# Performance work log

Hardware: AMD Instinct MI355X
Metric: run time of the kernel (lower is better)

Reference implementation:

```python
import jax, jax.numpy as jnp
import numpy as np

B, V, M, H = 256, 128, 256, 1024
TIMING_DIM = 10          # ceil(log2(max_timesteps=1024))
DECAY_ALPHA = 0.99
IN_DIM = (V + TIMING_DIM + 1 + 1) * M  # 35840


def setup_inputs() -> dict:
    key = jax.random.key(0)
    ks = jax.random.split(key, 12)
    x = jax.random.uniform(ks[0], (B, V), dtype=jnp.float32)
    memory = jax.random.uniform(ks[1], (B, M, V), dtype=jnp.float32)
    memory_timings = jax.random.randint(ks[2], (B, M), 0, 1000).astype(jnp.int64)
    memory_surprise = jax.random.uniform(ks[3], (B, M), dtype=jnp.float32)
    last_prediction = jax.random.uniform(ks[4], (B, V), dtype=jnp.float32)
    s1 = 1.0 / np.sqrt(IN_DIM)
    s2 = 1.0 / np.sqrt(H)
    W1 = jax.random.uniform(ks[5], (IN_DIM, H), dtype=jnp.float32, minval=-s1, maxval=s1)
    b1 = jnp.zeros((H,), jnp.float32)
    Wg = jax.random.uniform(ks[6], (IN_DIM, H), dtype=jnp.float32, minval=-s1, maxval=s1)
    bg = jnp.zeros((H,), jnp.float32)
    W2 = jax.random.uniform(ks[7], (H, V), dtype=jnp.float32, minval=-s2, maxval=s2)
    b2 = jnp.zeros((V,), jnp.float32)
    return {"x": x, "memory": memory, "memory_timings": memory_timings,
            "memory_surprise": memory_surprise, "last_prediction": last_prediction,
            "W1": W1, "b1": b1, "Wg": Wg, "bg": bg, "W2": W2, "b2": b2}


def _step(x, memory, memory_timings, memory_surprise, last_prediction):
    # surprise of incoming token under last prediction
    surprise = -jnp.log(jnp.sum(x * last_prediction, axis=1) + 1e-8)  # [B]
    # age + decay
    timings = memory_timings + 1
    surp = memory_surprise * DECAY_ALPHA
    # ring-buffer roll, write newest at slot 0
    mem = jnp.roll(memory, 1, axis=1).at[:, 0, :].set(x)
    timings = jnp.roll(timings, 1, axis=1).at[:, 0].set(0)
    surp = jnp.roll(surp, 1, axis=1).at[:, 0].set(surprise)
    # sort by age ascending, gather memory/surprise
    idx = jnp.argsort(timings, axis=1)                               # [B,M]
    sorted_timings = jnp.take_along_axis(timings, idx, axis=1)       # [B,M]
    sorted_memory = jnp.take_along_axis(mem, idx[..., None], axis=1)  # [B,M,V]
    sorted_surprise = jnp.take_along_axis(surp, idx, axis=1)          # [B,M]
    # binary encode timings
    powers = 2 ** jnp.arange(TIMING_DIM, dtype=sorted_timings.dtype)
    bits = ((sorted_timings[..., None] // powers) % 2).astype(jnp.float32)  # [B,M,T]
    norm_t = sorted_timings.astype(jnp.float32) / (
        jnp.max(sorted_timings, axis=1, keepdims=True).astype(jnp.float32) + 1.0)
    pred_input = jnp.concatenate(
        [sorted_memory.reshape(B, -1), bits.reshape(B, -1),
         norm_t.reshape(B, -1), sorted_surprise.reshape(B, -1)], axis=1)  # [B, IN_DIM]
    return pred_input


def reference(x, memory, memory_timings, memory_surprise, last_prediction,
              W1, b1, Wg, bg, W2, b2):
    pred_input = _step(x, memory, memory_timings, memory_surprise, last_prediction)
    # gated dense network: h = (xW1+b1) * sigmoid(xWg+bg); logits = hW2+b2
    h = (pred_input @ W1 + b1) * jax.nn.sigmoid(pred_input @ Wg + bg)
    return h @ W2 + b2
```

## Files before the change

kernel.cpp:

```cpp
#include <hip/hip_runtime.h>
#include <stdint.h>
#include <math.h>

#define BB 256
#define VV 128
#define MM 256
#define TDIM 10
#define HH 1024
#define IN_DIM 35840
#define KSPLIT 16
#define KSLICE 2240
#define BK 64
#define NCHUNK 35

using f32x4  = __attribute__((ext_vector_type(4))) float;
using bf16x8 = __attribute__((ext_vector_type(8))) short;

__device__ __forceinline__ unsigned short f2bf(float f) {
    unsigned int u = __float_as_uint(f);
    unsigned int r = (u + 0x7FFFu + ((u >> 16) & 1u)) >> 16;
    return (unsigned short)r;
}

__device__ __forceinline__ void gload_lds16(const void* g, void* l) {
    __builtin_amdgcn_global_load_lds(
        (const __attribute__((address_space(1))) unsigned int*)g,
        (__attribute__((address_space(3))) unsigned int*)l,
        16, 0, 0);
}

__global__ __launch_bounds__(256)
void k_build(const float* __restrict__ x, const float* __restrict__ memory,
             const int* __restrict__ timings, const float* __restrict__ msurp,
             const float* __restrict__ lastp, short* __restrict__ A)
{
    int b = blockIdx.x, t = threadIdx.x;
    __shared__ int t_s[MM], idx_s[MM], st_s[MM];
    __shared__ float red[MM];
    __shared__ float s_surprise;

    t_s[t] = (t == 0) ? 0 : timings[b*MM + t - 1] + 1;
    red[t] = (t < VV) ? x[b*VV + t] * lastp[b*VV + t] : 0.f;
    __syncthreads();
    for (int s = 128; s > 0; s >>= 1) {
        if (t < s) red[t] += red[t + s];
        __syncthreads();
    }
    if (t == 0) s_surprise = -logf(red[0] + 1e-8f);

    int ti = t_s[t], cnt = 0;
    #pragma unroll 4
    for (int j = 0; j < MM; ++j) {
        int tj = t_s[j];
        cnt += (tj < ti) || (tj == ti && j < t);
    }
    idx_s[cnt] = t;
    st_s[cnt]  = ti;
    __syncthreads();

    float invm = 1.f / ((float)st_s[MM-1] + 1.f);
    short* Ab = A + (size_t)b * IN_DIM;
    {
        int st = st_s[t], src = idx_s[t];
        #pragma unroll
        for (int tt = 0; tt < TDIM; ++tt)
            Ab[32768 + t*TDIM + tt] = (short)f2bf((float)((st >> tt) & 1));
        Ab[35328 + t] = (short)f2bf((float)st * invm);
        float sv = (src == 0) ? s_surprise : msurp[b*MM + src - 1] * 0.99f;
        Ab[35584 + t] = (short)f2bf(sv);
    }
    int half = t >> 7, v = t & (VV-1);
    for (int p = half; p < MM; p += 2) {
        int src = idx_s[p];
        float val = (src == 0) ? x[b*VV + v]
                               : memory[((size_t)b*MM + src - 1)*VV + v];
        Ab[p*VV + v] = (short)f2bf(val);
    }
}

__global__ __launch_bounds__(256)
void k_gemm(const short* __restrict__ A, const float* __restrict__ W1,
            const float* __restrict__ Wg, float* __restrict__ P)
{
    int ks = blockIdx.x;
    int xt = blockIdx.y;
    const float* W = (xt < 16) ? W1 : Wg;
    int wcol0 = (xt & 15) * 64;
    int pcol0 = xt * 64;
    int k0 = ks * KSLICE;

    __shared__ bf16x8 As8[2048];
    __shared__ bf16x8 Ws8[512];

    int t = threadIdx.x;
    int l = t & 63, wv = t >> 6;
    int r = l & 15, q = l >> 4;

    int aoff[4][2], boff[4][2];
    #pragma unroll
    for (int mt = 0; mt < 4; ++mt)
        #pragma unroll
        for (int s = 0; s < 2; ++s)
            aoff[mt][s] = (wv*64 + mt*16 + r)*8 + ((q + 4*s) ^ (r & 7));
    #pragma unroll
    for (int nt = 0; nt < 4; ++nt)
        #pragma unroll
        for (int s = 0; s < 2; ++s)
            boff[nt][s] = (nt*16 + r)*8 + ((q + 4*s) ^ (r & 7));

    f32x4 acc[4][4];
    #pragma unroll
    for (int mt = 0; mt < 4; ++mt)
        #pragma unroll
        for (int nt = 0; nt < 4; ++nt)
            acc[mt][nt] = (f32x4){0.f, 0.f, 0.f, 0.f};

    int wn  = t & 63;
    int wq4 = t >> 6;

    for (int c = 0; c < NCHUNK; ++c) {
        int kc = k0 + c*BK;
        __syncthreads();
        #pragma unroll
        for (int i = 0; i < 8; ++i) {
            int G = t + i*256;
            int m = G >> 3;
            int kb = (G & 7) ^ (m & 7);
            const short* gp = A + (size_t)m*IN_DIM + kc + kb*8;
            gload_lds16(gp, (void*)(As8 + ((t & ~63) + i*256)));
        }
        #pragma unroll
        for (int p4 = 0; p4 < 4; ++p4) {
            int kbase = p4*16 + wq4*4;
            const float* wp = W + (size_t)(kc + kbase)*HH + wcol0 + wn;
            float w0 = wp[0], w1 = wp[HH], w2 = wp[2*HH], w3 = wp[3*HH];
            unsigned int lo = (unsigned int)f2bf(w0) | ((unsigned int)f2bf(w1) << 16);
            unsigned int hi = (unsigned int)f2bf(w2) | ((unsigned int)f2bf(w3) << 16);
            int kb = kbase >> 3, hf = (kbase >> 2) & 1;
            unsigned int* dst = (unsigned int*)((short*)Ws8 +
                                ((wn*8 + (kb ^ (wn & 7)))*8 + hf*4));
            dst[0] = lo; dst[1] = hi;
        }
        __syncthreads();

        #pragma unroll
        for (int s = 0; s < 2; ++s) {
            bf16x8 af[4], bfr[4];
            #pragma unroll
            for (int mt = 0; mt < 4; ++mt) af[mt] = As8[aoff[mt][s]];
            #pragma unroll
            for (int nt = 0; nt < 4; ++nt) bfr[nt] = Ws8[boff[nt][s]];
            #pragma unroll
            for (int mt = 0; mt < 4; ++mt)
                #pragma unroll
                for (int nt = 0; nt < 4; ++nt)
                    acc[mt][nt] = __builtin_amdgcn_mfma_f32_16x16x32_bf16(
                        af[mt], bfr[nt], acc[mt][nt], 0, 0, 0);
        }
    }

    #pragma unroll
    for (int mt = 0; mt < 4; ++mt)
        #pragma unroll
        for (int nt = 0; nt < 4; ++nt)
            #pragma unroll
            for (int rg = 0; rg < 4; ++rg) {
                int m = wv*64 + mt*16 + q*4 + rg;
                int n = pcol0 + nt*16 + r;
                P[((size_t)ks*BB + m)*2048 + n] = acc[mt][nt][rg];
            }
}

__global__ __launch_bounds__(256)
void k_reduce(const float* __restrict__ P, const float* __restrict__ b1,
              const float* __restrict__ bg, float* __restrict__ h)
{
    int id = blockIdx.x * 256 + threadIdx.x;
    int b = id >> 10, j = id & 1023;
    float p1 = b1[j], pg = bg[j];
    #pragma unroll
    for (int ks = 0; ks < KSPLIT; ++ks) {
        size_t base = ((size_t)ks*BB + b)*2048;
        p1 += P[base + j];
        pg += P[base + 1024 + j];
    }
    float g = 1.f / (1.f + expf(-pg));
    h[(size_t)b*HH + j] = p1 * g;
}

__global__ __launch_bounds__(512)
void k_out(const float* __restrict__ h, const float* __restrict__ W2,
           const float* __restrict__ b2, float* __restrict__ out)
{
    int t = threadIdx.x;
    int v = t & 127, bi = t >> 7;
    int b = blockIdx.x * 4 + bi;
    const float* hb = h + (size_t)b*HH;
    float acc = b2[v];
    #pragma unroll 8
    for (int k = 0; k < HH; ++k)
        acc += hb[k] * W2[k*VV + v];
    out[(size_t)b*VV + v] = acc;
}

extern "C" void kernel_launch(void* const* d_in, const int* in_sizes, int n_in,
                              void* d_out, int out_size, void* d_ws, size_t ws_size,
                              hipStream_t stream)
{
    const float* x    = (const float*)d_in[0];
    const float* mem  = (const float*)d_in[1];
    const int*   tim  = (const int*)d_in[2];
    const float* msur = (const float*)d_in[3];
    const float* lp   = (const float*)d_in[4];
    const float* W1   = (const float*)d_in[5];
    const float* b1   = (const float*)d_in[6];
    const float* Wg   = (const float*)d_in[7];
    const float* bg   = (const float*)d_in[8];
    const float* W2   = (const float*)d_in[9];
    const float* b2   = (const float*)d_in[10];
    float* out = (float*)d_out;

    short* A = (short*)d_ws;
    float* P = (float*)((char*)d_ws + 18350080);
    float* h = (float*)((char*)d_ws + 51904512);

    k_build <<<256, 256, 0, stream>>>(x, mem, tim, msur, lp, A);
    k_gemm  <<<dim3(KSPLIT, 32), 256, 0, stream>>>(A, W1, Wg, P);
    k_reduce<<<1024, 256, 0, stream>>>(P, b1, bg, h);
    k_out   <<<64, 512, 0, stream>>>(h, W2, b2, out);
}
```

Measured before the change: 446.7 us.

## Narrow GEMM N-tile, prefetch weights into registers, split output GEMV over K

The main GEMM tile drops from 64 to 32 output columns, doubling the grid to 1024 blocks for more occupancy (launch_bounds now asks for 4 blocks per CU). Weight loads for the next K-chunk are issued into registers before the barrier, so global fp32 weight reads overlap with compute; each thread now loads 8 consecutive K rows and writes one 16-byte LDS vector. The A tile is now re-read from global twice as often because each block covers fewer columns. The final h@W2 kernel runs one block per batch row and splits K across two halves, combining them through shared memory, so the GEMV is spread over more blocks.

Result: no change. 439.6 us (-1.6%).

```diff
diff --git a/kernel.cpp b/kernel.cpp
--- a/kernel.cpp
+++ b/kernel.cpp
@@ -78,49 +78,61 @@
     }
 }
 
-__global__ __launch_bounds__(256)
+__global__ __launch_bounds__(256, 4)
 void k_gemm(const short* __restrict__ A, const float* __restrict__ W1,
             const float* __restrict__ Wg, float* __restrict__ P)
 {
     int ks = blockIdx.x;
     int xt = blockIdx.y;
-    const float* W = (xt < 16) ? W1 : Wg;
-    int wcol0 = (xt & 15) * 64;
-    int pcol0 = xt * 64;
+    const float* W = (xt < 32) ? W1 : Wg;
+    int wcol0 = (xt & 31) * 32;
+    int pcol0 = xt * 32;
     int k0 = ks * KSLICE;
 
     __shared__ bf16x8 As8[2048];
-    __shared__ bf16x8 Ws8[512];
+    __shared__ bf16x8 Ws8[256];
 
     int t = threadIdx.x;
     int l = t & 63, wv = t >> 6;
     int r = l & 15, q = l >> 4;
 
-    int aoff[4][2], boff[4][2];
+    int aoff[4][2], boff[2][2];
     #pragma unroll
     for (int mt = 0; mt < 4; ++mt)
         #pragma unroll
         for (int s = 0; s < 2; ++s)
             aoff[mt][s] = (wv*64 + mt*16 + r)*8 + ((q + 4*s) ^ (r & 7));
     #pragma unroll
-    for (int nt = 0; nt < 4; ++nt)
+    for (int nt = 0; nt < 2; ++nt)
         #pragma unroll
         for (int s = 0; s < 2; ++s)
             boff[nt][s] = (nt*16 + r)*8 + ((q + 4*s) ^ (r & 7));
 
-    f32x4 acc[4][4];
+    f32x4 acc[4][2];
     #pragma unroll
     for (int mt = 0; mt < 4; ++mt)
         #pragma unroll
-        for (int nt = 0; nt < 4; ++nt)
+        for (int nt = 0; nt < 2; ++nt)
             acc[mt][nt] = (f32x4){0.f, 0.f, 0.f, 0.f};
 
-    int wn  = t & 63;
-    int wq4 = t >> 6;
+    int wn = t & 31, wkg = t >> 5;
+    const float* wbase = W + (size_t)(k0 + wkg*8)*HH + wcol0 + wn;
+
+    float wreg[8];
+    #pragma unroll
+    for (int j = 0; j < 8; ++j) wreg[j] = wbase[(size_t)j*HH];
 
     for (int c = 0; c < NCHUNK; ++c) {
         int kc = k0 + c*BK;
         __syncthreads();
+        {
+            union { bf16x8 v; unsigned int d[4]; } u;
+            #pragma unroll
+            for (int j = 0; j < 4; ++j)
+                u.d[j] = (unsigned int)f2bf(wreg[2*j]) |
+                         ((unsigned int)f2bf(wreg[2*j+1]) << 16);
+            Ws8[wn*8 + (wkg ^ (wn & 7))] = u.v;
+        }
         #pragma unroll
         for (int i = 0; i < 8; ++i) {
             int G = t + i*256;
@@ -129,31 +141,25 @@
             const short* gp = A + (size_t)m*IN_DIM + kc + kb*8;
             gload_lds16(gp, (void*)(As8 + ((t & ~63) + i*256)));
         }
-        #pragma unroll
-        for (int p4 = 0; p4 < 4; ++p4) {
-            int kbase = p4*16 + wq4*4;
-            const float* wp = W + (size_t)(kc + kbase)*HH + wcol0 + wn;
-            float w0 = wp[0], w1 = wp[HH], w2 = wp[2*HH], w3 = wp[3*HH];
-            unsigned int lo = (unsigned int)f2bf(w0) | ((unsigned int)f2bf(w1) << 16);
-            unsigned int hi = (unsigned int)f2bf(w2) | ((unsigned int)f2bf(w3) << 16);
-            int kb = kbase >> 3, hf = (kbase >> 2) & 1;
-            unsigned int* dst = (unsigned int*)((short*)Ws8 +
-                                ((wn*8 + (kb ^ (wn & 7)))*8 + hf*4));
-            dst[0] = lo; dst[1] = hi;
+        {
+            int cn = (c + 1 < NCHUNK) ? c + 1 : c;
+            const float* wp = wbase + (size_t)cn*BK*HH;
+            #pragma unroll
+            for (int j = 0; j < 8; ++j) wreg[j] = wp[(size_t)j*HH];
         }
         __syncthreads();
 
         #pragma unroll
         for (int s = 0; s < 2; ++s) {
-            bf16x8 af[4], bfr[4];
+            bf16x8 af[4], bfr[2];
             #pragma unroll
             for (int mt = 0; mt < 4; ++mt) af[mt] = As8[aoff[mt][s]];
             #pragma unroll
-            for (int nt = 0; nt < 4; ++nt) bfr[nt] = Ws8[boff[nt][s]];
+            for (int nt = 0; nt < 2; ++nt) bfr[nt] = Ws8[boff[nt][s]];
             #pragma unroll
             for (int mt = 0; mt < 4; ++mt)
                 #pragma unroll
-                for (int nt = 0; nt < 4; ++nt)
+                for (int nt = 0; nt < 2; ++nt)
                     acc[mt][nt] = __builtin_amdgcn_mfma_f32_16x16x32_bf16(
                         af[mt], bfr[nt], acc[mt][nt], 0, 0, 0);
         }
@@ -162,7 +168,7 @@
     #pragma unroll
     for (int mt = 0; mt < 4; ++mt)
         #pragma unroll
-        for (int nt = 0; nt < 4; ++nt)
+        for (int nt = 0; nt < 2; ++nt)
             #pragma unroll
             for (int rg = 0; rg < 4; ++rg) {
                 int m = wv*64 + mt*16 + q*4 + rg;
@@ -188,19 +194,23 @@
     h[(size_t)b*HH + j] = p1 * g;
 }
 
-__global__ __launch_bounds__(512)
+__global__ __launch_bounds__(256)
 void k_out(const float* __restrict__ h, const float* __restrict__ W2,
            const float* __restrict__ b2, float* __restrict__ out)
 {
-    int t = threadIdx.x;
-    int v = t & 127, bi = t >> 7;
-    int b = blockIdx.x * 4 + bi;
-    const float* hb = h + (size_t)b*HH;
-    float acc = b2[v];
+    int b = blockIdx.x, t = threadIdx.x;
+    int v = t & 127, kh = t >> 7;
+    const float* hb = h + (size_t)b*HH + kh*512;
+    const float* wp = W2 + (size_t)kh*512*VV + v;
+    float acc = 0.f;
     #pragma unroll 8
-    for (int k = 0; k < HH; ++k)
-        acc += hb[k] * W2[k*VV + v];
-    out[(size_t)b*VV + v] = acc;
+    for (int k = 0; k < 512; ++k)
+        acc += hb[k] * wp[(size_t)k*VV];
+    __shared__ float s[256];
+    s[t] = acc;
+    __syncthreads();
+    if (t < 128)
+        out[(size_t)b*VV + v] = s[t] + s[t + 128] + b2[v];
 }
 
 extern "C" void kernel_launch(void* const* d_in, const int* in_sizes, int n_in,
@@ -225,7 +235,7 @@
     float* h = (float*)((char*)d_ws + 51904512);
 
     k_build <<<256, 256, 0, stream>>>(x, mem, tim, msur, lp, A);
-    k_gemm  <<<dim3(KSPLIT, 32), 256, 0, stream>>>(A, W1, Wg, P);
+    k_gemm  <<<dim3(KSPLIT, 64), 256, 0, stream>>>(A, W1, Wg, P);
     k_reduce<<<1024, 256, 0, stream>>>(P, b1, bg, h);
-    k_out   <<<64, 512, 0, stream>>>(h, W2, b2, out);
-}
+    k_out   <<<256, 256, 0, stream>>>(h, W2, b2, out);
+}
```
